# Kernel optimization log

Measured on AMD Instinct MI355X. Metric: run time of the kernel, lower is better.

Reference implementation:

```python
import jax, jax.numpy as jnp
import numpy as np

N_NODES = 100000
N_EDGES = 1600000
IN_DIM = 256
HID = 64
OUT_DIM = 1
N_GRAPHS = 100


def setup_inputs() -> dict:
    key = jax.random.key(0)
    ks = jax.random.split(key, 12)
    x = jax.random.normal(ks[0], (N_NODES, IN_DIM), dtype=jnp.float32)
    edge_index = jax.random.randint(ks[1], (2, N_EDGES), 0, N_NODES, dtype=jnp.int64 if jax.config.read('jax_enable_x64') else jnp.int32)
    batch = jnp.sort(jax.random.randint(ks[2], (N_NODES,), 0, N_GRAPHS, dtype=jnp.int32))
    def lin(k, fan_in, fan_out):
        bound = 1.0 / np.sqrt(fan_in)
        kw, kb = jax.random.split(k)
        W = jax.random.uniform(kw, (fan_in, fan_out), minval=-bound, maxval=bound, dtype=jnp.float32)
        b = jax.random.uniform(kb, (fan_out,), minval=-bound, maxval=bound, dtype=jnp.float32)
        return W, b
    W1, b1 = lin(ks[3], IN_DIM, HID)
    W2, b2 = lin(ks[4], HID, HID)
    W3, b3 = lin(ks[5], HID, HID)
    Wl, bl = lin(ks[6], HID, OUT_DIM)
    return {"x": x, "edge_index": edge_index, "batch": batch,
            "W1": W1, "b1": b1, "W2": W2, "b2": b2, "W3": W3, "b3": b3,
            "Wl": Wl, "bl": bl}


def _gcn_layer(h, src, dst, norm, W, b):
    # PyG GCNConv: h' = scatter_add(norm * (h @ W)[src] -> dst) + b
    h = h @ W                                   # [N, F_out]
    msg = h[src] * norm[:, None]                # [E+N, F_out] irregular gather
    agg = jax.ops.segment_sum(msg, dst, num_segments=N_NODES)
    return agg + b


def reference(x, edge_index, batch, W1, b1, W2, b2, W3, b3, Wl, bl):
    # add self loops (static shape) as GCNConv does by default
    loops = jnp.arange(N_NODES, dtype=edge_index.dtype)
    src = jnp.concatenate([edge_index[0], loops])  # [E+N]
    dst = jnp.concatenate([edge_index[1], loops])  # [E+N]
    # symmetric normalization: deg over targets incl. self loops
    deg = jax.ops.segment_sum(jnp.ones_like(dst, dtype=x.dtype), dst, num_segments=N_NODES)
    dinv = jnp.where(deg > 0, jax.lax.rsqrt(deg), 0.0)
    norm = dinv[src] * dinv[dst]                # [E+N]

    h = jax.nn.relu(_gcn_layer(x, src, dst, norm, W1, b1))
    h = jax.nn.relu(_gcn_layer(h, src, dst, norm, W2, b2))
    h = _gcn_layer(h, src, dst, norm, W3, b3)   # last conv: no relu

    # global_add_pool over graphs; dropout is identity at inference
    pooled = jax.ops.segment_sum(h, batch, num_segments=N_GRAPHS)  # [G, HID]
    return pooled @ Wl + bl                     # [G, 1]
```

## Files before the change

### kernel.cpp

```cpp
#include <hip/hip_runtime.h>

#define N_NODES 100000
#define N_EDGES 1600000
#define IN_DIM 256
#define HID 64
#define N_GRAPHS 100
#define BSHIFT 8
#define NBUCK 391
#define CHUNK 4096
#define BCAP 5120

typedef __attribute__((ext_vector_type(8))) short short8;
typedef __attribute__((ext_vector_type(8))) unsigned short us8;
typedef __attribute__((ext_vector_type(4))) float floatx4;
typedef __attribute__((ext_vector_type(2))) float floatx2;

__device__ __forceinline__ unsigned short f2b(float f) {
    unsigned int u = __float_as_uint(f);
    unsigned int r = (u + 0x7FFFu + ((u >> 16) & 1u)) >> 16;
    return (unsigned short)r;
}
__device__ __forceinline__ float b2f(unsigned short b) {
    return __uint_as_float(((unsigned int)b) << 16);
}
__device__ __forceinline__ unsigned char f2e4m3(float f) {
    return (unsigned char)(__builtin_amdgcn_cvt_pk_fp8_f32(f, 0.f, 0, false) & 0xFF);
}


__global__ void k_prep(const float* __restrict__ W1, const float* __restrict__ W2,
                       const float* __restrict__ W3, const float* __restrict__ Wl,
                       const float* __restrict__ b3,
                       unsigned short* __restrict__ wt1, unsigned short* __restrict__ wt2,
                       float* __restrict__ w3l,
                       int* __restrict__ bcnt, float* __restrict__ partial) {
    int i = blockIdx.x * 256 + threadIdx.x;
    if (i < IN_DIM * HID) {
        int k = i >> 6, n = i & 63;
        wt1[n * IN_DIM + k] = f2b(W1[i]);
    }
    if (i < HID * HID) {
        int k = i >> 6, n = i & 63;
        wt2[n * HID + k] = f2b(W2[i]);
    }
    if (i < NBUCK) bcnt[i] = 0;
    if (i < N_GRAPHS * 256) partial[i] = 0.f;
    if (blockIdx.x == 0) {
        int t = threadIdx.x;
        if (t < HID) {
            float s = 0.f;
            for (int n = 0; n < HID; ++n) s += W3[t * HID + n] * Wl[n];
            w3l[t] = s;
        } else if (t == HID) {
            float s = 0.f;
            for (int n = 0; n < HID; ++n) s += b3[n] * Wl[n];
            w3l[HID] = s;
        }
    }
}


__global__ __launch_bounds__(256) void k_scatter(const int* __restrict__ src,
                                                 const int* __restrict__ dst,
                                                 int* __restrict__ bcnt,
                                                 int* __restrict__ ebuckF) {
    __shared__ int lc[NBUCK];
    const int b = blockIdx.x, t = threadIdx.x;
    for (int i = t; i < NBUCK; i += 256) lc[i] = 0;
    __syncthreads();
    const int base = b * CHUNK;
    int pk[16], bk[16], rk[16];
#pragma unroll
    for (int i = 0; i < 16; ++i) {
        int e = base + i * 256 + t;
        rk[i] = -1;
        if (e < N_EDGES) {
            int s = src[e], d = dst[e];
            bk[i] = d >> BSHIFT;
            pk[i] = (s << BSHIFT) | (d & 255);
            rk[i] = atomicAdd(&lc[bk[i]], 1);
        }
    }
    __syncthreads();
    for (int i = t; i < NBUCK; i += 256)
        lc[i] = lc[i] ? atomicAdd(&bcnt[i], lc[i]) : 0;
    __syncthreads();
#pragma unroll
    for (int i = 0; i < 16; ++i)
        if (rk[i] >= 0) {
            int p = lc[bk[i]] + rk[i];
            if (p < BCAP) ebuckF[bk[i] * BCAP + p] = pk[i];
        }
}


__global__ __launch_bounds__(256) void k_dgemm1(const int* __restrict__ bcnt,
                                                const int* __restrict__ ebuckF,
                                                int* __restrict__ deg,
                                                float* __restrict__ dinv,
                                                int* __restrict__ rowptr,
                                                int* __restrict__ colF,
                                                const float* __restrict__ X,
                                                const unsigned short* __restrict__ Wt,
                                                unsigned char* __restrict__ Tb8) {
    __shared__ unsigned short Wb[64][264];
    const int t = threadIdx.x;

    if (blockIdx.x < NBUCK) {
        int* ld = (int*)&Wb[0][0];
        int* sA = ld + 256;
        int* lf = sA + 256;
        const int b = blockIdx.x;
        const int cnt = min(bcnt[b], BCAP);
        const int ebase = b * BCAP;
        ld[t] = 1;
        __syncthreads();
        for (int j = t; j < cnt; j += 256) atomicAdd(&ld[ebuckF[ebase + j] & 255], 1);
        __syncthreads();
        const int node = (b << BSHIFT) + t;
        const int dg = ld[t];
        if (node < N_NODES) {
            deg[node] = dg;
            dinv[node] = rsqrtf((float)dg);
        }
        const int c = (node < N_NODES) ? dg - 1 : 0;
        sA[t] = c;
        __syncthreads();
        for (int off = 1; off < 256; off <<= 1) {
            int u = (t >= off) ? sA[t - off] : 0;
            __syncthreads();
            sA[t] += u;
            __syncthreads();
        }
        const int pos = ebase + sA[t] - c;
        if (node < N_NODES) rowptr[node] = pos;
        lf[t] = pos;
        __syncthreads();
        for (int j = t; j < cnt; j += 256) {
            int v = ebuckF[ebase + j];
            int p = atomicAdd(&lf[v & 255], 1);
            colF[p] = v >> BSHIFT;
        }
        return;
    }

    const int lane = t & 63, wv = t >> 6;
    const int fl = lane & 15, quad = lane >> 4;
    const int r0 = (blockIdx.x - NBUCK) * 64;

    for (int g = t; g < 64 * 32; g += 256) {
        int n = g >> 5, kc8 = g & 31;
        *(us8*)&Wb[n][kc8 * 8] = *(const us8*)(Wt + n * IN_DIM + kc8 * 8);
    }

    const int arow = r0 + wv * 16 + fl;
    const bool valid = arow < N_NODES;
    const float* xp = X + (size_t)(valid ? arow : 0) * IN_DIM;

    floatx4 acc[4];
#pragma unroll
    for (int j = 0; j < 4; ++j) acc[j] = (floatx4){0.f, 0.f, 0.f, 0.f};

    __syncthreads();

#pragma unroll
    for (int kc = 0; kc < IN_DIM; kc += 32) {
        float4 x0 = make_float4(0.f, 0.f, 0.f, 0.f);
        float4 x1 = make_float4(0.f, 0.f, 0.f, 0.f);
        if (valid) {
            x0 = *(const float4*)(xp + kc + quad * 8);
            x1 = *(const float4*)(xp + kc + quad * 8 + 4);
        }
        short8 a;
        a[0] = (short)f2b(x0.x); a[1] = (short)f2b(x0.y);
        a[2] = (short)f2b(x0.z); a[3] = (short)f2b(x0.w);
        a[4] = (short)f2b(x1.x); a[5] = (short)f2b(x1.y);
        a[6] = (short)f2b(x1.z); a[7] = (short)f2b(x1.w);
#pragma unroll
        for (int ct = 0; ct < 4; ++ct) {
            short8 b = *(const short8*)&Wb[ct * 16 + fl][kc + quad * 8];
            acc[ct] = __builtin_amdgcn_mfma_f32_16x16x32_bf16(a, b, acc[ct], 0, 0, 0);
        }
    }

    int rbase = r0 + wv * 16 + quad * 4;
#pragma unroll
    for (int r = 0; r < 4; ++r) {
        int row = rbase + r;
        if (row < N_NODES) {
#pragma unroll
            for (int ct = 0; ct < 4; ++ct)
                Tb8[(size_t)row * HID + ct * 16 + fl] = f2e4m3(acc[ct][r]);
        }
    }
}


__global__ __launch_bounds__(1024) void k_aggmm2(const unsigned char* __restrict__ Tb8,
                                                 const int* __restrict__ rowptr,
                                                 const int* __restrict__ deg,
                                                 const float* __restrict__ dinv,
                                                 const int* __restrict__ col,
                                                 const float* __restrict__ bias,
                                                 const unsigned short* __restrict__ Wt,
                                                 unsigned char* __restrict__ Tb2_8) {
    __shared__ unsigned short Wb[64][72];
    __shared__ unsigned short Hs[16][72];
    const int t = threadIdx.x;
    const int lane = t & 63, wv = t >> 6;
    const int grp = lane >> 3, fl8 = lane & 7;

    for (int g = t; g < 64 * 8; g += 1024) {
        int n = g >> 3, kc8 = g & 7;
        *(us8*)&Wb[n][kc8 * 8] = *(const us8*)(Wt + n * HID + kc8 * 8);
    }

    const int node = blockIdx.x * 16 + wv;
    int e = __builtin_amdgcn_readfirstlane(rowptr[node]);
    const int end = e + __builtin_amdgcn_readfirstlane(deg[node]) - 1;
    const float di = dinv[node];
    float a0 = 0.f, a1 = 0.f, a2 = 0.f, a3 = 0.f;
    float a4 = 0.f, a5 = 0.f, a6 = 0.f, a7 = 0.f;

#define ACC_FP8(dv, vx, vy)                                                 \
    {                                                                       \
        floatx2 p0 = __builtin_amdgcn_cvt_pk_f32_fp8((int)(vx), false);     \
        floatx2 p1 = __builtin_amdgcn_cvt_pk_f32_fp8((int)(vx), true);      \
        floatx2 p2 = __builtin_amdgcn_cvt_pk_f32_fp8((int)(vy), false);     \
        floatx2 p3 = __builtin_amdgcn_cvt_pk_f32_fp8((int)(vy), true);      \
        a0 = fmaf(dv, p0.x, a0); a1 = fmaf(dv, p0.y, a1);                   \
        a2 = fmaf(dv, p1.x, a2); a3 = fmaf(dv, p1.y, a3);                   \
        a4 = fmaf(dv, p2.x, a4); a5 = fmaf(dv, p2.y, a5);                   \
        a6 = fmaf(dv, p3.x, a6); a7 = fmaf(dv, p3.y, a7);                   \
    }

    for (; e + 16 <= end; e += 16) {
        int s0 = col[e + grp];
        int s1 = col[e + 8 + grp];
        float dv0 = dinv[s0], dv1 = dinv[s1];
        uint2 t0 = *(const uint2*)(Tb8 + (size_t)s0 * HID + fl8 * 8);
        uint2 t1 = *(const uint2*)(Tb8 + (size_t)s1 * HID + fl8 * 8);
        ACC_FP8(dv0, t0.x, t0.y);
        ACC_FP8(dv1, t1.x, t1.y);
    }
    for (; e + 8 <= end; e += 8) {
        int s = col[e + grp];
        float dv = dinv[s];
        uint2 tv = *(const uint2*)(Tb8 + (size_t)s * HID + fl8 * 8);
        ACC_FP8(dv, tv.x, tv.y);
    }
    if (e + grp < end) {
        int s = col[e + grp];
        float dv = dinv[s];
        uint2 tv = *(const uint2*)(Tb8 + (size_t)s * HID + fl8 * 8);
        ACC_FP8(dv, tv.x, tv.y);
    }
    a0 += __shfl_xor(a0, 8);  a1 += __shfl_xor(a1, 8);
    a2 += __shfl_xor(a2, 8);  a3 += __shfl_xor(a3, 8);
    a4 += __shfl_xor(a4, 8);  a5 += __shfl_xor(a5, 8);
    a6 += __shfl_xor(a6, 8);  a7 += __shfl_xor(a7, 8);
    a0 += __shfl_xor(a0, 16); a1 += __shfl_xor(a1, 16);
    a2 += __shfl_xor(a2, 16); a3 += __shfl_xor(a3, 16);
    a4 += __shfl_xor(a4, 16); a5 += __shfl_xor(a5, 16);
    a6 += __shfl_xor(a6, 16); a7 += __shfl_xor(a7, 16);
    a0 += __shfl_xor(a0, 32); a1 += __shfl_xor(a1, 32);
    a2 += __shfl_xor(a2, 32); a3 += __shfl_xor(a3, 32);
    a4 += __shfl_xor(a4, 32); a5 += __shfl_xor(a5, 32);
    a6 += __shfl_xor(a6, 32); a7 += __shfl_xor(a7, 32);
    {
        uint2 sv = *(const uint2*)(Tb8 + (size_t)node * HID + fl8 * 8);
        ACC_FP8(di, sv.x, sv.y);
    }
#undef ACC_FP8
    float4 b0 = *(const float4*)(bias + fl8 * 8);
    float4 b1v = *(const float4*)(bias + fl8 * 8 + 4);
    a0 = fmaxf(fmaf(di, a0, b0.x), 0.f);
    a1 = fmaxf(fmaf(di, a1, b0.y), 0.f);
    a2 = fmaxf(fmaf(di, a2, b0.z), 0.f);
    a3 = fmaxf(fmaf(di, a3, b0.w), 0.f);
    a4 = fmaxf(fmaf(di, a4, b1v.x), 0.f);
    a5 = fmaxf(fmaf(di, a5, b1v.y), 0.f);
    a6 = fmaxf(fmaf(di, a6, b1v.z), 0.f);
    a7 = fmaxf(fmaf(di, a7, b1v.w), 0.f);
    if (grp == 0) {
        us8 o;
        o[0] = f2b(a0); o[1] = f2b(a1); o[2] = f2b(a2); o[3] = f2b(a3);
        o[4] = f2b(a4); o[5] = f2b(a5); o[6] = f2b(a6); o[7] = f2b(a7);
        *(us8*)&Hs[wv][fl8 * 8] = o;
    }
    __syncthreads();

    if (wv == 0) {
        const int fl = lane & 15, quad = lane >> 4;
        floatx4 acc[4];
#pragma unroll
        for (int j = 0; j < 4; ++j) acc[j] = (floatx4){0.f, 0.f, 0.f, 0.f};
#pragma unroll
        for (int kc = 0; kc < HID; kc += 32) {
            short8 a = *(const short8*)&Hs[fl][kc + quad * 8];
#pragma unroll
            for (int ct = 0; ct < 4; ++ct) {
                short8 b = *(const short8*)&Wb[ct * 16 + fl][kc + quad * 8];
                acc[ct] = __builtin_amdgcn_mfma_f32_16x16x32_bf16(a, b, acc[ct], 0, 0, 0);
            }
        }
        int rbase = blockIdx.x * 16 + quad * 4;
#pragma unroll
        for (int r = 0; r < 4; ++r) {
            int row = rbase + r;
            float di2 = dinv[row];
#pragma unroll
            for (int ct = 0; ct < 4; ++ct)
                Tb2_8[(size_t)row * HID + ct * 16 + fl] = f2e4m3(di2 * acc[ct][r]);
        }
    }
}

#define ACC8(vx, vy)                                                    \
    {                                                                   \
        floatx2 p0 = __builtin_amdgcn_cvt_pk_f32_fp8((int)(vx), false); \
        floatx2 p1 = __builtin_amdgcn_cvt_pk_f32_fp8((int)(vx), true);  \
        floatx2 p2 = __builtin_amdgcn_cvt_pk_f32_fp8((int)(vy), false); \
        floatx2 p3 = __builtin_amdgcn_cvt_pk_f32_fp8((int)(vy), true);  \
        a0 += p0.x; a1 += p0.y; a2 += p1.x; a3 += p1.y;                 \
        a4 += p2.x; a5 += p2.y; a6 += p3.x; a7 += p3.y;                 \
    }


__global__ __launch_bounds__(1024) void k_agg_z(const unsigned char* __restrict__ Tb8,
                                                const int* __restrict__ rowptr,
                                                const int* __restrict__ deg,
                                                const float* __restrict__ dinv,
                                                const int* __restrict__ col,
                                                const float* __restrict__ bias,
                                                const float* __restrict__ w3l,
                                                float* __restrict__ z) {
    int lane = threadIdx.x & 63;
    int node = blockIdx.x * 16 + (threadIdx.x >> 6);
    int grp = lane >> 3, fl = lane & 7;
    int e = __builtin_amdgcn_readfirstlane(rowptr[node]);
    int end = e + __builtin_amdgcn_readfirstlane(deg[node]) - 1;
    float a0 = 0.f, a1 = 0.f, a2 = 0.f, a3 = 0.f;
    float a4 = 0.f, a5 = 0.f, a6 = 0.f, a7 = 0.f;
    for (; e + 16 <= end; e += 16) {
        int s0 = col[e + grp];
        int s1 = col[e + 8 + grp];
        uint2 t0 = *(const uint2*)(Tb8 + (size_t)s0 * HID + fl * 8);
        uint2 t1 = *(const uint2*)(Tb8 + (size_t)s1 * HID + fl * 8);
        ACC8(t0.x, t0.y);
        ACC8(t1.x, t1.y);
    }
    for (; e + 8 <= end; e += 8) {
        int s = col[e + grp];
        uint2 tv = *(const uint2*)(Tb8 + (size_t)s * HID + fl * 8);
        ACC8(tv.x, tv.y);
    }
    if (e + grp < end) {
        int s = col[e + grp];
        uint2 tv = *(const uint2*)(Tb8 + (size_t)s * HID + fl * 8);
        ACC8(tv.x, tv.y);
    }
    a0 += __shfl_xor(a0, 8);  a1 += __shfl_xor(a1, 8);
    a2 += __shfl_xor(a2, 8);  a3 += __shfl_xor(a3, 8);
    a4 += __shfl_xor(a4, 8);  a5 += __shfl_xor(a5, 8);
    a6 += __shfl_xor(a6, 8);  a7 += __shfl_xor(a7, 8);
    a0 += __shfl_xor(a0, 16); a1 += __shfl_xor(a1, 16);
    a2 += __shfl_xor(a2, 16); a3 += __shfl_xor(a3, 16);
    a4 += __shfl_xor(a4, 16); a5 += __shfl_xor(a5, 16);
    a6 += __shfl_xor(a6, 16); a7 += __shfl_xor(a7, 16);
    a0 += __shfl_xor(a0, 32); a1 += __shfl_xor(a1, 32);
    a2 += __shfl_xor(a2, 32); a3 += __shfl_xor(a3, 32);
    a4 += __shfl_xor(a4, 32); a5 += __shfl_xor(a5, 32);
    a6 += __shfl_xor(a6, 32); a7 += __shfl_xor(a7, 32);
    {
        uint2 sv = *(const uint2*)(Tb8 + (size_t)node * HID + fl * 8);
        ACC8(sv.x, sv.y);
    }
    float di = dinv[node];
    float4 b0 = *(const float4*)(bias + fl * 8);
    float4 b1v = *(const float4*)(bias + fl * 8 + 4);
    a0 = fmaxf(fmaf(di, a0, b0.x), 0.f);
    a1 = fmaxf(fmaf(di, a1, b0.y), 0.f);
    a2 = fmaxf(fmaf(di, a2, b0.z), 0.f);
    a3 = fmaxf(fmaf(di, a3, b0.w), 0.f);
    a4 = fmaxf(fmaf(di, a4, b1v.x), 0.f);
    a5 = fmaxf(fmaf(di, a5, b1v.y), 0.f);
    a6 = fmaxf(fmaf(di, a6, b1v.z), 0.f);
    a7 = fmaxf(fmaf(di, a7, b1v.w), 0.f);
    float4 w0 = *(const float4*)(w3l + fl * 8);
    float4 w1v = *(const float4*)(w3l + fl * 8 + 4);
    float s = a0 * w0.x + a1 * w0.y + a2 * w0.z + a3 * w0.w +
              a4 * w1v.x + a5 * w1v.y + a6 * w1v.z + a7 * w1v.w;
    s += __shfl_xor(s, 1);
    s += __shfl_xor(s, 2);
    s += __shfl_xor(s, 4);
    if (lane == 0) z[node] = di * s;
}
#undef ACC8

__global__ __launch_bounds__(256) void k_aggpool_s(const float* __restrict__ z,
                                                   const int* __restrict__ rowptr,
                                                   const int* __restrict__ deg,
                                                   const float* __restrict__ dinv,
                                                   const int* __restrict__ col,
                                                   const float* __restrict__ w3l,
                                                   const int* __restrict__ batch,
                                                   float* __restrict__ partial) {
    int i = blockIdx.x * 256 + threadIdx.x;
    if (i >= N_NODES) return;
    int e = rowptr[i];
    int end = e + deg[i] - 1;
    float s0 = z[i], s1 = 0.f, s2 = 0.f, s3 = 0.f;
    for (; e + 4 <= end; e += 4) {
        s0 += z[col[e]];
        s1 += z[col[e + 1]];
        s2 += z[col[e + 2]];
        s3 += z[col[e + 3]];
    }
    for (; e < end; ++e) s0 += z[col[e]];
    float s = w3l[HID] + dinv[i] * (s0 + s1 + s2 + s3);
    atomicAdd(&partial[batch[i] * 256 + (blockIdx.x & 255)], s);
}

__global__ void k_pool_reduce(const float* __restrict__ partial,
                              const float* __restrict__ bl,
                              float* __restrict__ out) {
    int g = blockIdx.x, t = threadIdx.x;
    float s = partial[g * 256 + t];
    s += __shfl_xor(s, 32);
    s += __shfl_xor(s, 16);
    s += __shfl_xor(s, 8);
    s += __shfl_xor(s, 4);
    s += __shfl_xor(s, 2);
    s += __shfl_xor(s, 1);
    __shared__ float ws[4];
    if ((t & 63) == 0) ws[t >> 6] = s;
    __syncthreads();
    if (t == 0) out[g] = bl[0] + ws[0] + ws[1] + ws[2] + ws[3];
}

extern "C" void kernel_launch(void* const* d_in, const int* in_sizes, int n_in,
                              void* d_out, int out_size, void* d_ws, size_t ws_size,
                              hipStream_t stream) {
    const float* x     = (const float*)d_in[0];
    const int*   ei    = (const int*)d_in[1];
    const int*   batch = (const int*)d_in[2];
    const float* W1    = (const float*)d_in[3];
    const float* b1    = (const float*)d_in[4];
    const float* W2    = (const float*)d_in[5];
    const float* b2    = (const float*)d_in[6];
    const float* W3    = (const float*)d_in[7];
    const float* b3    = (const float*)d_in[8];
    const float* Wl    = (const float*)d_in[9];
    const float* bl    = (const float*)d_in[10];
    float* out = (float*)d_out;

    char* p = (char*)d_ws;
    unsigned char*  tb8 = (unsigned char*)p;  p += (size_t)N_NODES * HID;
    unsigned char*  hB8 = (unsigned char*)p;  p += (size_t)N_NODES * HID;
    int*   colF    = (int*)p;   p += (size_t)NBUCK * BCAP * 4;
    int*   ebuckF  = (int*)p;   p += (size_t)NBUCK * BCAP * 4;
    int*   deg     = (int*)p;   p += (size_t)N_NODES * 4;
    float* dinv    = (float*)p; p += (size_t)N_NODES * 4;
    int*   rowptr  = (int*)p;   p += (size_t)N_NODES * 4;
    float* z       = (float*)p; p += (size_t)N_NODES * 4;
    int*   bcnt    = (int*)p;   p += (NBUCK + 1) * 4;
    float* partial = (float*)p; p += (size_t)N_GRAPHS * 256 * 4;
    unsigned short* wt1 = (unsigned short*)p; p += (size_t)IN_DIM * HID * 2;
    unsigned short* wt2 = (unsigned short*)p; p += (size_t)HID * HID * 2;
    float* w3l     = (float*)p; p += 128 * 4;

    const int* src  = ei;
    const int* dstp = ei + N_EDGES;

    const int nb = (N_NODES + 255) / 256;
    const int cb = (N_EDGES + CHUNK - 1) / CHUNK;
    const int gemm_blocks = (N_NODES + 63) / 64;
    const int agg_blocks = N_NODES / 16;

    k_prep<<<128, 256, 0, stream>>>(W1, W2, W3, Wl, b3, wt1, wt2, w3l, bcnt, partial);
    k_scatter<<<cb, 256, 0, stream>>>(src, dstp, bcnt, ebuckF);
    k_dgemm1<<<NBUCK + gemm_blocks, 256, 0, stream>>>(bcnt, ebuckF, deg, dinv, rowptr,
                                                      colF, x, wt1, tb8);

    k_aggmm2<<<agg_blocks, 1024, 0, stream>>>(tb8, rowptr, deg, dinv, colF, b1, wt2, hB8);
    k_agg_z<<<agg_blocks, 1024, 0, stream>>>(hB8, rowptr, deg, dinv, colF, b2, w3l, z);

    k_aggpool_s<<<nb, 256, 0, stream>>>(z, rowptr, deg, dinv, colF, w3l, batch, partial);
    k_pool_reduce<<<N_GRAPHS, 256, 0, stream>>>(partial, bl, out);
}
```

Baseline: 349.0 us.

## Co-schedule edge scatter with first GEMM and fuse pooling reduction into output

The edge bucketing scatter now runs in the same launch as the first-layer GEMM, using otherwise idle blocks. This lets the latency-bound scatter overlap the bandwidth-bound feature transform. Degree, rowptr and CSR fill move into a separate kernel that runs after. The final pooling accumulates per-graph sums in shared memory and atomically adds into the output, which is pre-initialized with the bias. That removes the partial buffer and the separate reduce kernel, at the cost of global float atomics with a nondeterministic summation order.

```diff
diff --git a/kernel.cpp b/kernel.cpp
--- a/kernel.cpp
+++ b/kernel.cpp
@@ -28,12 +28,17 @@
 }
 
 
-__global__ void k_prep(const float* __restrict__ W1, const float* __restrict__ W2,
-                       const float* __restrict__ W3, const float* __restrict__ Wl,
-                       const float* __restrict__ b3,
-                       unsigned short* __restrict__ wt1, unsigned short* __restrict__ wt2,
-                       float* __restrict__ w3l,
-                       int* __restrict__ bcnt, float* __restrict__ partial) {
+__global__ __launch_bounds__(256) void k_prep(const float* __restrict__ W1,
+                                              const float* __restrict__ W2,
+                                              const float* __restrict__ W3,
+                                              const float* __restrict__ Wl,
+                                              const float* __restrict__ b3,
+                                              const float* __restrict__ bl,
+                                              unsigned short* __restrict__ wt1,
+                                              unsigned short* __restrict__ wt2,
+                                              float* __restrict__ w3l,
+                                              int* __restrict__ bcnt,
+                                              float* __restrict__ out) {
     int i = blockIdx.x * 256 + threadIdx.x;
     if (i < IN_DIM * HID) {
         int k = i >> 6, n = i & 63;
@@ -44,7 +49,7 @@
         wt2[n * HID + k] = f2b(W2[i]);
     }
     if (i < NBUCK) bcnt[i] = 0;
-    if (i < N_GRAPHS * 256) partial[i] = 0.f;
+    if (i < N_GRAPHS) out[i] = bl[0];
     if (blockIdx.x == 0) {
         int t = threadIdx.x;
         if (t < HID) {
@@ -60,46 +65,10 @@
 }
 
 
-__global__ __launch_bounds__(256) void k_scatter(const int* __restrict__ src,
-                                                 const int* __restrict__ dst,
-                                                 int* __restrict__ bcnt,
-                                                 int* __restrict__ ebuckF) {
-    __shared__ int lc[NBUCK];
-    const int b = blockIdx.x, t = threadIdx.x;
-    for (int i = t; i < NBUCK; i += 256) lc[i] = 0;
-    __syncthreads();
-    const int base = b * CHUNK;
-    int pk[16], bk[16], rk[16];
-#pragma unroll
-    for (int i = 0; i < 16; ++i) {
-        int e = base + i * 256 + t;
-        rk[i] = -1;
-        if (e < N_EDGES) {
-            int s = src[e], d = dst[e];
-            bk[i] = d >> BSHIFT;
-            pk[i] = (s << BSHIFT) | (d & 255);
-            rk[i] = atomicAdd(&lc[bk[i]], 1);
-        }
-    }
-    __syncthreads();
-    for (int i = t; i < NBUCK; i += 256)
-        lc[i] = lc[i] ? atomicAdd(&bcnt[i], lc[i]) : 0;
-    __syncthreads();
-#pragma unroll
-    for (int i = 0; i < 16; ++i)
-        if (rk[i] >= 0) {
-            int p = lc[bk[i]] + rk[i];
-            if (p < BCAP) ebuckF[bk[i] * BCAP + p] = pk[i];
-        }
-}
-
-
-__global__ __launch_bounds__(256) void k_dgemm1(const int* __restrict__ bcnt,
-                                                const int* __restrict__ ebuckF,
-                                                int* __restrict__ deg,
-                                                float* __restrict__ dinv,
-                                                int* __restrict__ rowptr,
-                                                int* __restrict__ colF,
+__global__ __launch_bounds__(256) void k_sgemm1(const int* __restrict__ src,
+                                                const int* __restrict__ dst,
+                                                int* __restrict__ bcnt,
+                                                int* __restrict__ ebuckF,
                                                 const float* __restrict__ X,
                                                 const unsigned short* __restrict__ Wt,
                                                 unsigned char* __restrict__ Tb8) {
@@ -107,40 +76,33 @@
     const int t = threadIdx.x;
 
     if (blockIdx.x < NBUCK) {
-        int* ld = (int*)&Wb[0][0];
-        int* sA = ld + 256;
-        int* lf = sA + 256;
+        int* lc = (int*)&Wb[0][0];
         const int b = blockIdx.x;
-        const int cnt = min(bcnt[b], BCAP);
-        const int ebase = b * BCAP;
-        ld[t] = 1;
+        for (int i = t; i < NBUCK; i += 256) lc[i] = 0;
         __syncthreads();
-        for (int j = t; j < cnt; j += 256) atomicAdd(&ld[ebuckF[ebase + j] & 255], 1);
+        const int base = b * CHUNK;
+        int pk[16], bk[16], rk[16];
+#pragma unroll
+        for (int i = 0; i < 16; ++i) {
+            int e = base + i * 256 + t;
+            rk[i] = -1;
+            if (e < N_EDGES) {
+                int s = src[e], d = dst[e];
+                bk[i] = d >> BSHIFT;
+                pk[i] = (s << BSHIFT) | (d & 255);
+                rk[i] = atomicAdd(&lc[bk[i]], 1);
+            }
+        }
         __syncthreads();
-        const int node = (b << BSHIFT) + t;
-        const int dg = ld[t];
-        if (node < N_NODES) {
-            deg[node] = dg;
-            dinv[node] = rsqrtf((float)dg);
-        }
-        const int c = (node < N_NODES) ? dg - 1 : 0;
-        sA[t] = c;
+        for (int i = t; i < NBUCK; i += 256)
+            lc[i] = lc[i] ? atomicAdd(&bcnt[i], lc[i]) : 0;
         __syncthreads();
-        for (int off = 1; off < 256; off <<= 1) {
-            int u = (t >= off) ? sA[t - off] : 0;
-            __syncthreads();
-            sA[t] += u;
-            __syncthreads();
-        }
-        const int pos = ebase + sA[t] - c;
-        if (node < N_NODES) rowptr[node] = pos;
-        lf[t] = pos;
-        __syncthreads();
-        for (int j = t; j < cnt; j += 256) {
-            int v = ebuckF[ebase + j];
-            int p = atomicAdd(&lf[v & 255], 1);
-            colF[p] = v >> BSHIFT;
-        }
+#pragma unroll
+        for (int i = 0; i < 16; ++i)
+            if (rk[i] >= 0) {
+                int p = lc[bk[i]] + rk[i];
+                if (p < BCAP) ebuckF[bk[i] * BCAP + p] = pk[i];
+            }
         return;
     }
 
@@ -192,6 +154,49 @@
             for (int ct = 0; ct < 4; ++ct)
                 Tb8[(size_t)row * HID + ct * 16 + fl] = f2e4m3(acc[ct][r]);
         }
+    }
+}
+
+
+__global__ __launch_bounds__(256) void k_degfill(const int* __restrict__ bcnt,
+                                                 const int* __restrict__ ebuckF,
+                                                 int* __restrict__ deg,
+                                                 float* __restrict__ dinv,
+                                                 int* __restrict__ rowptr,
+                                                 int* __restrict__ colF) {
+    __shared__ int ld[256];
+    __shared__ int sA[256];
+    __shared__ int lf[256];
+    const int b = blockIdx.x, t = threadIdx.x;
+    const int cnt = min(bcnt[b], BCAP);
+    const int ebase = b * BCAP;
+    ld[t] = 1;
+    __syncthreads();
+    for (int j = t; j < cnt; j += 256) atomicAdd(&ld[ebuckF[ebase + j] & 255], 1);
+    __syncthreads();
+    const int node = (b << BSHIFT) + t;
+    const int dg = ld[t];
+    if (node < N_NODES) {
+        deg[node] = dg;
+        dinv[node] = rsqrtf((float)dg);
+    }
+    const int c = (node < N_NODES) ? dg - 1 : 0;
+    sA[t] = c;
+    __syncthreads();
+    for (int off = 1; off < 256; off <<= 1) {
+        int u = (t >= off) ? sA[t - off] : 0;
+        __syncthreads();
+        sA[t] += u;
+        __syncthreads();
+    }
+    const int pos = ebase + sA[t] - c;
+    if (node < N_NODES) rowptr[node] = pos;
+    lf[t] = pos;
+    __syncthreads();
+    for (int j = t; j < cnt; j += 256) {
+        int v = ebuckF[ebase + j];
+        int p = atomicAdd(&lf[v & 255], 1);
+        colF[p] = v >> BSHIFT;
     }
 }
 
@@ -398,45 +403,49 @@
 }
 #undef ACC8
 
-__global__ __launch_bounds__(256) void k_aggpool_s(const float* __restrict__ z,
-                                                   const int* __restrict__ rowptr,
-                                                   const int* __restrict__ deg,
-                                                   const float* __restrict__ dinv,
-                                                   const int* __restrict__ col,
-                                                   const float* __restrict__ w3l,
-                                                   const int* __restrict__ batch,
-                                                   float* __restrict__ partial) {
-    int i = blockIdx.x * 256 + threadIdx.x;
-    if (i >= N_NODES) return;
-    int e = rowptr[i];
-    int end = e + deg[i] - 1;
-    float s0 = z[i], s1 = 0.f, s2 = 0.f, s3 = 0.f;
-    for (; e + 4 <= end; e += 4) {
-        s0 += z[col[e]];
-        s1 += z[col[e + 1]];
-        s2 += z[col[e + 2]];
-        s3 += z[col[e + 3]];
-    }
-    for (; e < end; ++e) s0 += z[col[e]];
-    float s = w3l[HID] + dinv[i] * (s0 + s1 + s2 + s3);
-    atomicAdd(&partial[batch[i] * 256 + (blockIdx.x & 255)], s);
-}
-
-__global__ void k_pool_reduce(const float* __restrict__ partial,
-                              const float* __restrict__ bl,
-                              float* __restrict__ out) {
-    int g = blockIdx.x, t = threadIdx.x;
-    float s = partial[g * 256 + t];
-    s += __shfl_xor(s, 32);
-    s += __shfl_xor(s, 16);
-    s += __shfl_xor(s, 8);
-    s += __shfl_xor(s, 4);
-    s += __shfl_xor(s, 2);
-    s += __shfl_xor(s, 1);
-    __shared__ float ws[4];
-    if ((t & 63) == 0) ws[t >> 6] = s;
-    __syncthreads();
-    if (t == 0) out[g] = bl[0] + ws[0] + ws[1] + ws[2] + ws[3];
+
+__global__ __launch_bounds__(256) void k_aggpool(const float* __restrict__ z,
+                                                 const int* __restrict__ rowptr,
+                                                 const int* __restrict__ deg,
+                                                 const float* __restrict__ dinv,
+                                                 const int* __restrict__ col,
+                                                 const float* __restrict__ w3l,
+                                                 const int* __restrict__ batch,
+                                                 float* __restrict__ out) {
+    __shared__ float gacc[16];
+    __shared__ int gbase_s;
+    const int t = threadIdx.x;
+    const int i = blockIdx.x * 256 + t;
+    if (t < 16) gacc[t] = 0.f;
+    if (t == 0) {
+        int bi = blockIdx.x * 256;
+        if (bi > N_NODES - 1) bi = N_NODES - 1;
+        gbase_s = batch[bi];
+    }
+    __syncthreads();
+    const int gbase = gbase_s;
+    if (i < N_NODES) {
+        int e = rowptr[i];
+        int end = e + deg[i] - 1;
+        float s0 = z[i], s1 = 0.f, s2 = 0.f, s3 = 0.f;
+        for (; e + 4 <= end; e += 4) {
+            s0 += z[col[e]];
+            s1 += z[col[e + 1]];
+            s2 += z[col[e + 2]];
+            s3 += z[col[e + 3]];
+        }
+        for (; e < end; ++e) s0 += z[col[e]];
+        float s = w3l[HID] + dinv[i] * (s0 + s1 + s2 + s3);
+        int g = batch[i];
+        int off = g - gbase;
+        if (off >= 0 && off < 16) atomicAdd(&gacc[off], s);
+        else atomicAdd(&out[g], s);
+    }
+    __syncthreads();
+    if (t < 16) {
+        int g = gbase + t;
+        if (g < N_GRAPHS && gacc[t] != 0.f) atomicAdd(&out[g], gacc[t]);
+    }
 }
 
 extern "C" void kernel_launch(void* const* d_in, const int* in_sizes, int n_in,
@@ -465,7 +474,6 @@
     int*   rowptr  = (int*)p;   p += (size_t)N_NODES * 4;
     float* z       = (float*)p; p += (size_t)N_NODES * 4;
     int*   bcnt    = (int*)p;   p += (NBUCK + 1) * 4;
-    float* partial = (float*)p; p += (size_t)N_GRAPHS * 256 * 4;
     unsigned short* wt1 = (unsigned short*)p; p += (size_t)IN_DIM * HID * 2;
     unsigned short* wt2 = (unsigned short*)p; p += (size_t)HID * HID * 2;
     float* w3l     = (float*)p; p += 128 * 4;
@@ -478,14 +486,12 @@
     const int gemm_blocks = (N_NODES + 63) / 64;
     const int agg_blocks = N_NODES / 16;
 
-    k_prep<<<128, 256, 0, stream>>>(W1, W2, W3, Wl, b3, wt1, wt2, w3l, bcnt, partial);
-    k_scatter<<<cb, 256, 0, stream>>>(src, dstp, bcnt, ebuckF);
-    k_dgemm1<<<NBUCK + gemm_blocks, 256, 0, stream>>>(bcnt, ebuckF, deg, dinv, rowptr,
-                                                      colF, x, wt1, tb8);
+    k_prep<<<128, 256, 0, stream>>>(W1, W2, W3, Wl, b3, bl, wt1, wt2, w3l, bcnt, out);
+    k_sgemm1<<<cb + gemm_blocks, 256, 0, stream>>>(src, dstp, bcnt, ebuckF, x, wt1, tb8);
+    k_degfill<<<NBUCK, 256, 0, stream>>>(bcnt, ebuckF, deg, dinv, rowptr, colF);
 
     k_aggmm2<<<agg_blocks, 1024, 0, stream>>>(tb8, rowptr, deg, dinv, colF, b1, wt2, hB8);
     k_agg_z<<<agg_blocks, 1024, 0, stream>>>(hB8, rowptr, deg, dinv, colF, b2, w3l, z);
 
-    k_aggpool_s<<<nb, 256, 0, stream>>>(z, rowptr, deg, dinv, colF, w3l, batch, partial);
-    k_pool_reduce<<<N_GRAPHS, 256, 0, stream>>>(partial, bl, out);
-}
+    k_aggpool<<<nb, 256, 0, stream>>>(z, rowptr, deg, dinv, colF, w3l, batch, out);
+}
```

After: 332.5 us, median of 2. 4.7% less time.
